# Performance work log

Hardware: AMD Instinct MI355X
Metric: run time of the kernel (lower is better)

Reference implementation:

```python
import jax, jax.numpy as jnp
import numpy as np

DIM_K = 64
DIM_V = 64
MODEL_DIM = 1024


def setup_inputs() -> dict:
    key = jax.random.key(0)
    ks = jax.random.split(key, 9)
    B, T, C = 4, 4096, MODEL_DIM
    scale = 1.0 / np.sqrt(C)
    return {
        "Q": jax.random.normal(ks[0], (B, T, C), dtype=jnp.float32),
        "K": jax.random.normal(ks[1], (B, T, C), dtype=jnp.float32),
        "V": jax.random.normal(ks[2], (B, T, C), dtype=jnp.float32),
        "Wq": jax.random.normal(ks[3], (C, DIM_K), dtype=jnp.float32) * scale,
        "bq": jax.random.normal(ks[4], (DIM_K,), dtype=jnp.float32) * 0.02,
        "Wk": jax.random.normal(ks[5], (C, DIM_K), dtype=jnp.float32) * scale,
        "bk": jax.random.normal(ks[6], (DIM_K,), dtype=jnp.float32) * 0.02,
        "Wv": jax.random.normal(ks[7], (C, DIM_V), dtype=jnp.float32) * scale,
        "bv": jax.random.normal(ks[8], (DIM_V,), dtype=jnp.float32) * 0.02,
    }


def reference(Q, K, V, Wq, bq, Wk, bk, Wv, bv):
    # Linear projections: [B,T,C] @ [C,dk] -> [B,T,dk]
    q = jnp.einsum("btc,cd->btd", Q, Wq) + bq
    k = jnp.einsum("btc,cd->btd", K, Wk) + bk
    v = jnp.einsum("btc,cd->btd", V, Wv) + bv
    T = q.shape[1]
    # Scaled dot-product scores [B,T,T], causal mask, softmax (dropout p=0 -> identity)
    scores = jnp.einsum("bqd,bkd->bqk", q, k) / jnp.sqrt(jnp.float32(DIM_K))
    causal = jnp.tril(jnp.ones((T, T), dtype=bool))
    scores = jnp.where(causal, scores, -jnp.inf)
    weights = jax.nn.softmax(scores, axis=-1)
    return jnp.einsum("bqk,bkd->bqd", weights, v)
```

## Files before the change

### kernel.cpp

```cpp
#include <hip/hip_runtime.h>
#include <hip/hip_bf16.h>
#include <cstdint>
#include <cstddef>


typedef __attribute__((ext_vector_type(8))) short short8;
typedef __attribute__((ext_vector_type(4))) float f32x4;
typedef __attribute__((ext_vector_type(4))) unsigned int uint4v;
typedef __attribute__((ext_vector_type(4))) unsigned short ushort4v;
typedef unsigned short ushort;

#define MFMA16x16x32(A,B,C) __builtin_amdgcn_mfma_f32_16x16x32_bf16((A),(B),(C),0,0,0)

static __device__ __forceinline__ unsigned pack2_bf16(float f0, float f1){
  unsigned u0 = __builtin_bit_cast(unsigned, f0) + 0x8000u;
  unsigned u1 = __builtin_bit_cast(unsigned, f1) + 0x8000u;
  return __builtin_amdgcn_perm(u1, u0, 0x07060302u);
}
static __device__ __forceinline__ unsigned short bf16u(float f){
  return (unsigned short)((__builtin_bit_cast(unsigned, f) + 0x8000u) >> 16);
}
static __device__ __forceinline__ short8 cvt8(f32x4 a, f32x4 b){
  union { unsigned u[4]; short8 s; } r;
  r.u[0] = pack2_bf16(a[0], a[1]);
  r.u[1] = pack2_bf16(a[2], a[3]);
  r.u[2] = pack2_bf16(b[0], b[1]);
  r.u[3] = pack2_bf16(b[2], b[3]);
  return r.s;
}
static __device__ __forceinline__ float fast_exp2(float x){
  float r; asm("v_exp_f32 %0, %1" : "=v"(r) : "v"(x)); return r;
}
static __device__ __forceinline__ float fast_rcp(float x){
  float r; asm("v_rcp_f32 %0, %1" : "=v"(r) : "v"(x)); return r;
}
static __device__ __forceinline__ void gl_lds16(const ushort* g, ushort* l){
  __builtin_amdgcn_global_load_lds(
      (const __attribute__((address_space(1))) void*)g,
      (__attribute__((address_space(3))) void*)l, 16, 0, 0);
}

__global__ __launch_bounds__(256) void pack_w(
    const float* __restrict__ Wq, const float* __restrict__ Wk,
    const float* __restrict__ Wv, unsigned short* __restrict__ Wp,
    float* __restrict__ out, float* __restrict__ Lbuf)
{
  int t = blockIdx.x * 256 + threadIdx.x;
  if (t < 24576){
    int lane = t & 63, nf = (t >> 6) & 3, cc = (t >> 8) & 31, p = t >> 13;
    int qd = lane >> 4, l = lane & 15;
    const float* W = (p == 0) ? Wq : ((p == 1) ? Wk : Wv);
    const float* src = W + (size_t)(cc * 32 + qd * 8) * 64 + nf * 16 + l;
    uint4v u;
    #pragma unroll
    for (int j = 0; j < 4; ++j)
      u[j] = pack2_bf16(src[(2 * j) * 64], src[(2 * j + 1) * 64]);
    *(uint4v*)(Wp + (size_t)t * 8) = u;
  }
  const f32x4 z = (f32x4){0.f, 0.f, 0.f, 0.f};
  f32x4* o4 = (f32x4*)out;
  f32x4* l4 = (f32x4*)Lbuf;
  for (int i = t; i < 262144 + 4096; i += 65536){
    if (i < 262144) o4[i] = z;
    else l4[i - 262144] = z;
  }
}

__global__ __launch_bounds__(256) void proj_gemm(
    const float* __restrict__ Qx, const float* __restrict__ Kx, const float* __restrict__ Vx,
    const float* __restrict__ bqp, const float* __restrict__ bkp, const float* __restrict__ bvp,
    const unsigned short* __restrict__ Wp,
    unsigned short* __restrict__ qb, unsigned short* __restrict__ kb,
    unsigned short* __restrict__ vt)
{
  const int tid = threadIdx.x;
  const int lane = tid & 63, wid = tid >> 6;
  const int qd = lane >> 4, l = lane & 15;
  const int p = blockIdx.y;
  const float* X = (p == 0) ? Qx : ((p == 1) ? Kx : Vx);
  const float* bias = (p == 0) ? bqp : ((p == 1) ? bkp : bvp);
  const unsigned short* W = Wp + (size_t)p * 65536;

  const int row0 = blockIdx.x * 64 + wid * 16;
  const float* xa = X + (size_t)(row0 + l) * 1024 + qd * 8;
  const unsigned short* wb = W + (size_t)lane * 8;

  f32x4 acc[4];
  #pragma unroll
  for (int nf = 0; nf < 4; ++nf) acc[nf] = (f32x4){0.f, 0.f, 0.f, 0.f};

  #pragma unroll 4
  for (int cc = 0; cc < 32; ++cc){
    f32x4 al = *(const f32x4*)(xa + cc * 32);
    f32x4 ah = *(const f32x4*)(xa + cc * 32 + 4);
    const unsigned short* wc = wb + (size_t)cc * 2048;
    short8 b0 = *(const short8*)(wc);
    short8 b1 = *(const short8*)(wc + 512);
    short8 b2 = *(const short8*)(wc + 1024);
    short8 b3 = *(const short8*)(wc + 1536);
    short8 a = cvt8(al, ah);
    acc[0] = MFMA16x16x32(a, b0, acc[0]);
    acc[1] = MFMA16x16x32(a, b1, acc[1]);
    acc[2] = MFMA16x16x32(a, b2, acc[2]);
    acc[3] = MFMA16x16x32(a, b3, acc[3]);
  }

  if (p == 2){
    int tg = row0 + qd * 4;
    int b = tg >> 12, tl = tg & 4095;
    #pragma unroll
    for (int nf = 0; nf < 4; ++nf){
      float bb = bias[nf * 16 + l];
      ushort4v pk;
      #pragma unroll
      for (int r = 0; r < 4; ++r) pk[r] = bf16u(acc[nf][r] + bb);
      *(ushort4v*)(vt + ((size_t)b * 64 + nf * 16 + l) * 4096 + tl) = pk;
    }
  } else {
    unsigned short* o = (p == 0) ? qb : kb;
    #pragma unroll
    for (int nf = 0; nf < 4; ++nf){
      float bb = bias[nf * 16 + l];
      #pragma unroll
      for (int r = 0; r < 4; ++r){
        int row = row0 + qd * 4 + r;
        o[(size_t)row * 64 + nf * 16 + l] = bf16u(acc[nf][r] + bb);
      }
    }
  }
}

#define K1 0.18033688011112042f

__global__ __launch_bounds__(256) void flash_split(
    const ushort* __restrict__ qb, const ushort* __restrict__ kb,
    const ushort* __restrict__ vt, float* __restrict__ out,
    float* __restrict__ Lbuf)
{
  __shared__ ushort Ks[2][4096];
  __shared__ ushort Vs[2][4096];
  __shared__ ushort pbuf[4][16 * 40];

  const int tid = threadIdx.x;
  const int lane = tid & 63, wid = tid >> 6;
  const int qd = lane >> 4, l = lane & 15;
  const int lw = l & 7;

  int bidx = (int)blockIdx.x;
  const int batch = bidx & 3;
  int j = 287 - (bidx >> 2);
  int g = 0;
  while (j >= 4 * (g + 1) * (g + 2)) ++g;
  int j2 = j - 4 * g * (g + 1);
  int tq = j2 / (g + 1);
  int s = j2 - tq * (g + 1);
  const int q0b = (8 * g + tq) * 64;
  const int kvstart = s * 512;
  const int kvend = min(kvstart + 512, q0b + 64);
  const int q0w = q0b + wid * 16;

  const ushort* kbB = kb + (size_t)batch * 262144;
  const ushort* vtB = vt + (size_t)batch * 262144;

  const ushort* qrow = qb + ((size_t)(batch * 4096 + q0w + l)) * 64 + qd * 8;
  short8 Qf0 = *(const short8*)(qrow);
  short8 Qf1 = *(const short8*)(qrow + 32);

  const f32x4 Zc = (f32x4){0.f, 0.f, 0.f, 0.f};
  f32x4 Oc[4] = {Zc, Zc, Zc, Zc};
  f32x4 Lacc = Zc;
  short8 onesf;
  #pragma unroll
  for (int i = 0; i < 8; ++i) onesf[i] = (short)0x3F80;

  ushort* pw = &pbuf[wid][0];
  ushort* pwr = pw + qd * 160 + l;
  const ushort* prd = pw + l * 40 + qd * 8;

#define STAGE(BB, KVC) do{                                                     \
    int r8_ = lane >> 3, sw_ = ((lane & 7) ^ r8_) << 3;                        \
    int rA_ = wid * 8 + r8_;                                                   \
    const ushort* gk_ = kbB + (size_t)((KVC) + rA_) * 64 + sw_;                \
    gl_lds16(gk_,            &Ks[BB][wid * 512]);                              \
    gl_lds16(gk_ + 32 * 64,  &Ks[BB][2048 + wid * 512]);                       \
    const ushort* gv_ = vtB + (size_t)rA_ * 4096 + (KVC) + sw_;                \
    gl_lds16(gv_,              &Vs[BB][wid * 512]);                            \
    gl_lds16(gv_ + 32 * 4096,  &Vs[BB][2048 + wid * 512]);                     \
  } while (0)

#define CHUNK(BB, ROFF, KVG) do{                                               \
    if ((KVG) < q0w + 16){                                                     \
      const ushort* KsB_ = &Ks[BB][0];                                         \
      const ushort* VsB_ = &Vs[BB][0];                                         \
      short8 k0_ = *(const short8*)(KsB_ + (l + (ROFF)) * 64 + ((qd ^ lw) << 3));        \
      short8 k1_ = *(const short8*)(KsB_ + (l + (ROFF)) * 64 + (((qd + 4) ^ lw) << 3));  \
      short8 k2_ = *(const short8*)(KsB_ + (l + 16 + (ROFF)) * 64 + ((qd ^ lw) << 3));   \
      short8 k3_ = *(const short8*)(KsB_ + (l + 16 + (ROFF)) * 64 + (((qd + 4) ^ lw) << 3)); \
      f32x4 s0_ = MFMA16x16x32(Qf0, k0_, Zc);                                  \
      s0_ = MFMA16x16x32(Qf1, k1_, s0_);                                       \
      f32x4 s1_ = MFMA16x16x32(Qf0, k2_, Zc);                                  \
      s1_ = MFMA16x16x32(Qf1, k3_, s1_);                                       \
      float p0_[4], p1_[4];                                                    \
      _Pragma("unroll")                                                        \
      for (int r = 0; r < 4; ++r){                                             \
        p0_[r] = fast_exp2(s0_[r] * K1);                                       \
        p1_[r] = fast_exp2(s1_[r] * K1);                                       \
      }                                                                        \
      if ((KVG) + 31 > q0w){                                                   \
        _Pragma("unroll")                                                      \
        for (int r = 0; r < 4; ++r){                                           \
          int q_ = q0w + qd * 4 + r;                                           \
          if ((KVG) + l > q_) p0_[r] = 0.f;                                    \
          if ((KVG) + 16 + l > q_) p1_[r] = 0.f;                               \
        }                                                                      \
      }                                                                        \
      _Pragma("unroll")                                                        \
      for (int r = 0; r < 4; ++r){                                             \
        pwr[r * 40] = bf16u(p0_[r]);                                           \
        pwr[r * 40 + 16] = bf16u(p1_[r]);                                      \
      }                                                                        \
      short8 Pf_ = *(const short8*)(prd);                                      \
      int vs_ = ((qd + ((ROFF) >> 3)) ^ lw) << 3;                              \
      short8 v0_ = *(const short8*)(VsB_ + (l     ) * 64 + vs_);               \
      short8 v1_ = *(const short8*)(VsB_ + (l + 16) * 64 + vs_);               \
      short8 v2_ = *(const short8*)(VsB_ + (l + 32) * 64 + vs_);               \
      short8 v3_ = *(const short8*)(VsB_ + (l + 48) * 64 + vs_);               \
      Lacc = MFMA16x16x32(Pf_, onesf, Lacc);                                   \
      Oc[0] = MFMA16x16x32(Pf_, v0_, Oc[0]);                                   \
      Oc[1] = MFMA16x16x32(Pf_, v1_, Oc[1]);                                   \
      Oc[2] = MFMA16x16x32(Pf_, v2_, Oc[2]);                                   \
      Oc[3] = MFMA16x16x32(Pf_, v3_, Oc[3]);                                   \
    }                                                                          \
  } while (0)

  const int nst = (kvend - kvstart) >> 6;
  STAGE(0, kvstart);
  __syncthreads();
  int kvc = kvstart;
  for (int it = 0; it < nst; ++it){
    int bb = it & 1;
    if (it + 1 < nst) STAGE(bb ^ 1, kvc + 64);
    CHUNK(bb, 0, kvc);
    CHUNK(bb, 32, kvc + 32);
    __syncthreads();
    kvc += 64;
  }
#undef STAGE
#undef CHUNK

  float* ob = out + ((size_t)(batch * 4096 + q0w + qd * 4)) * 64 + l;
  #pragma unroll
  for (int nf = 0; nf < 4; ++nf)
    #pragma unroll
    for (int r = 0; r < 4; ++r)
      atomicAdd(&ob[(size_t)r * 64 + nf * 16], Oc[nf][r]);
  if (l == 0){
    float* lb = Lbuf + batch * 4096 + q0w + qd * 4;
    #pragma unroll
    for (int r = 0; r < 4; ++r) atomicAdd(&lb[r], Lacc[r]);
  }
}

__global__ __launch_bounds__(256) void normalize(
    float* __restrict__ out, const float* __restrict__ Lbuf)
{
  int idx = blockIdx.x * 256 + threadIdx.x;
  f32x4 v = ((f32x4*)out)[idx];
  float inv = fast_rcp(Lbuf[idx >> 4]);
  v[0] *= inv; v[1] *= inv; v[2] *= inv; v[3] *= inv;
  ((f32x4*)out)[idx] = v;
}

extern "C" void kernel_launch(void* const* d_in, const int* in_sizes, int n_in,
                              void* d_out, int out_size, void* d_ws, size_t ws_size,
                              hipStream_t stream)
{
  const float* Q  = (const float*)d_in[0];
  const float* K  = (const float*)d_in[1];
  const float* V  = (const float*)d_in[2];
  const float* Wq = (const float*)d_in[3];
  const float* bq = (const float*)d_in[4];
  const float* Wk = (const float*)d_in[5];
  const float* bk = (const float*)d_in[6];
  const float* Wv = (const float*)d_in[7];
  const float* bv = (const float*)d_in[8];
  float* out = (float*)d_out;

  unsigned short* qb   = (unsigned short*)d_ws;
  unsigned short* kbuf = qb + (size_t)16384 * 64;
  unsigned short* vtp  = kbuf + (size_t)16384 * 64;
  unsigned short* Wp   = vtp + (size_t)16384 * 64;
  float* Lbuf = (float*)(Wp + (size_t)3 * 65536);

  pack_w<<<256, 256, 0, stream>>>(Wq, Wk, Wv, Wp, out, Lbuf);
  proj_gemm<<<dim3(256, 3), 256, 0, stream>>>(Q, K, V, bq, bk, bv, Wp, qb, kbuf, vtp);
  flash_split<<<1152, 256, 0, stream>>>(qb, kbuf, vtp, out, Lbuf);
  normalize<<<1024, 256, 0, stream>>>(out, Lbuf);
}
```

Measured before the change: 254.7 us.

## Stage projection inputs through LDS with double-buffered async loads; unroll flash loop by two

The projection GEMM now copies X tiles into swizzled, double-buffered LDS using global_load_lds and prefetches the next chunk of packed weights into registers. Explicit vmcnt waits overlap each load with the MFMAs on the current chunk. The goal is to hide global memory latency in this bandwidth-heavy fp32 input read. In the flash kernel the ping-pong buffers become separate static arrays and the loop is unrolled by two, so buffer selection is resolved at compile time and no longer needs runtime indexing. The tradeoff is more LDS and register pressure in proj_gemm, and the hand-written waitcnt counts must match the exact number of outstanding loads.

```diff
diff --git a/kernel.cpp b/kernel.cpp
--- a/kernel.cpp
+++ b/kernel.cpp
@@ -34,7 +34,7 @@
 static __device__ __forceinline__ float fast_rcp(float x){
   float r; asm("v_rcp_f32 %0, %1" : "=v"(r) : "v"(x)); return r;
 }
-static __device__ __forceinline__ void gl_lds16(const ushort* g, ushort* l){
+static __device__ __forceinline__ void gl_lds16(const void* g, void* l){
   __builtin_amdgcn_global_load_lds(
       (const __attribute__((address_space(1))) void*)g,
       (__attribute__((address_space(3))) void*)l, 16, 0, 0);
@@ -73,6 +73,9 @@
     unsigned short* __restrict__ qb, unsigned short* __restrict__ kb,
     unsigned short* __restrict__ vt)
 {
+  __shared__ float Xs0[4096];
+  __shared__ float Xs1[4096];
+
   const int tid = threadIdx.x;
   const int lane = tid & 63, wid = tid >> 6;
   const int qd = lane >> 4, l = lane & 15;
@@ -82,28 +85,90 @@
   const unsigned short* W = Wp + (size_t)p * 65536;
 
   const int row0 = blockIdx.x * 64 + wid * 16;
-  const float* xa = X + (size_t)(row0 + l) * 1024 + qd * 8;
+  const float* Xrow = X + (size_t)row0 * 1024;
   const unsigned short* wb = W + (size_t)lane * 8;
+
+  float* s0 = Xs0 + wid * 1024;
+  float* s1 = Xs1 + wid * 1024;
+  const float* r0 = s0 + l * 64;
+  const float* r1 = s1 + l * 64;
 
   f32x4 acc[4];
   #pragma unroll
   for (int nf = 0; nf < 4; ++nf) acc[nf] = (f32x4){0.f, 0.f, 0.f, 0.f};
 
-  #pragma unroll 4
-  for (int cc = 0; cc < 32; ++cc){
-    f32x4 al = *(const f32x4*)(xa + cc * 32);
-    f32x4 ah = *(const f32x4*)(xa + cc * 32 + 4);
-    const unsigned short* wc = wb + (size_t)cc * 2048;
-    short8 b0 = *(const short8*)(wc);
-    short8 b1 = *(const short8*)(wc + 512);
-    short8 b2 = *(const short8*)(wc + 1024);
-    short8 b3 = *(const short8*)(wc + 1536);
-    short8 a = cvt8(al, ah);
-    acc[0] = MFMA16x16x32(a, b0, acc[0]);
-    acc[1] = MFMA16x16x32(a, b1, acc[1]);
-    acc[2] = MFMA16x16x32(a, b2, acc[2]);
-    acc[3] = MFMA16x16x32(a, b3, acc[3]);
-  }
+  short8 wA0, wA1, wA2, wA3, wA4, wA5, wA6, wA7;
+  short8 wB0, wB1, wB2, wB3, wB4, wB5, wB6, wB7;
+
+#define PSTAGE(DST, CK) do{                                                    \
+    _Pragma("unroll")                                                          \
+    for (int j_ = 0; j_ < 4; ++j_){                                            \
+      int rr_ = j_ * 4 + qd;                                    \
+      int ss_ = l ^ rr_;                                  \
+      gl_lds16(Xrow + (size_t)rr_ * 1024 + (CK) * 64 + (ss_ << 2),             \
+               (DST) + j_ * 256);                                              \
+    }                                                                          \
+  } while (0)
+
+#define WLOADM(S, CK) do{                                                      \
+    const unsigned short* wc_ = wb + (size_t)(CK) * 4096;                      \
+    w##S##0 = *(const short8*)(wc_);                                           \
+    w##S##1 = *(const short8*)(wc_ + 512);                                     \
+    w##S##2 = *(const short8*)(wc_ + 1024);                                    \
+    w##S##3 = *(const short8*)(wc_ + 1536);                                    \
+    w##S##4 = *(const short8*)(wc_ + 2048);                                    \
+    w##S##5 = *(const short8*)(wc_ + 2560);                                    \
+    w##S##6 = *(const short8*)(wc_ + 3072);                                    \
+    w##S##7 = *(const short8*)(wc_ + 3584);                                    \
+  } while (0)
+
+#define PCOMP(RD, S) do{                                                       \
+    {                                                                          \
+      int sb_ = qd * 2;                                                        \
+      f32x4 al_ = *(const f32x4*)((RD) + ((sb_ ^ l) << 2));                    \
+      f32x4 ah_ = *(const f32x4*)((RD) + (((sb_ + 1) ^ l) << 2));              \
+      short8 a_ = cvt8(al_, ah_);                                              \
+      acc[0] = MFMA16x16x32(a_, w##S##0, acc[0]);                              \
+      acc[1] = MFMA16x16x32(a_, w##S##1, acc[1]);                              \
+      acc[2] = MFMA16x16x32(a_, w##S##2, acc[2]);                              \
+      acc[3] = MFMA16x16x32(a_, w##S##3, acc[3]);                              \
+    }                                                                          \
+    {                                                                          \
+      int sb_ = 8 + qd * 2;                                                    \
+      f32x4 al_ = *(const f32x4*)((RD) + ((sb_ ^ l) << 2));                    \
+      f32x4 ah_ = *(const f32x4*)((RD) + (((sb_ + 1) ^ l) << 2));              \
+      short8 a_ = cvt8(al_, ah_);                                              \
+      acc[0] = MFMA16x16x32(a_, w##S##4, acc[0]);                              \
+      acc[1] = MFMA16x16x32(a_, w##S##5, acc[1]);                              \
+      acc[2] = MFMA16x16x32(a_, w##S##6, acc[2]);                              \
+      acc[3] = MFMA16x16x32(a_, w##S##7, acc[3]);                              \
+    }                                                                          \
+  } while (0)
+
+#define VW12 do{ asm volatile("s_waitcnt vmcnt(12)" ::: "memory");             \
+                 __builtin_amdgcn_sched_barrier(0); } while (0)
+#define VW0  do{ asm volatile("s_waitcnt vmcnt(0)"  ::: "memory");             \
+                 __builtin_amdgcn_sched_barrier(0); } while (0)
+
+  PSTAGE(s0, 0);
+  WLOADM(A, 0);
+  #pragma unroll
+  for (int h = 0; h < 16; ++h){
+    if ((h & 1) == 0){
+      if (h + 1 < 16){ PSTAGE(s1, h + 1); WLOADM(B, h + 1); VW12; }
+      else           { VW0; }
+      PCOMP(r0, A);
+    } else {
+      if (h + 1 < 16){ PSTAGE(s0, h + 1); WLOADM(A, h + 1); VW12; }
+      else           { VW0; }
+      PCOMP(r1, B);
+    }
+  }
+#undef PSTAGE
+#undef WLOADM
+#undef PCOMP
+#undef VW12
+#undef VW0
 
   if (p == 2){
     int tg = row0 + qd * 4;
@@ -137,8 +202,10 @@
     const ushort* __restrict__ vt, float* __restrict__ out,
     float* __restrict__ Lbuf)
 {
-  __shared__ ushort Ks[2][4096];
-  __shared__ ushort Vs[2][4096];
+  __shared__ ushort Ks0[4096];
+  __shared__ ushort Ks1[4096];
+  __shared__ ushort Vs0[4096];
+  __shared__ ushort Vs1[4096];
   __shared__ ushort pbuf[4][16 * 40];
 
   const int tid = threadIdx.x;
@@ -177,21 +244,21 @@
   ushort* pwr = pw + qd * 160 + l;
   const ushort* prd = pw + l * 40 + qd * 8;
 
-#define STAGE(BB, KVC) do{                                                     \
+#define STAGE(KA, VA, KVC) do{                                                 \
     int r8_ = lane >> 3, sw_ = ((lane & 7) ^ r8_) << 3;                        \
     int rA_ = wid * 8 + r8_;                                                   \
     const ushort* gk_ = kbB + (size_t)((KVC) + rA_) * 64 + sw_;                \
-    gl_lds16(gk_,            &Ks[BB][wid * 512]);                              \
-    gl_lds16(gk_ + 32 * 64,  &Ks[BB][2048 + wid * 512]);                       \
+    gl_lds16(gk_,            &(KA)[wid * 512]);                                \
+    gl_lds16(gk_ + 32 * 64,  &(KA)[2048 + wid * 512]);                         \
     const ushort* gv_ = vtB + (size_t)rA_ * 4096 + (KVC) + sw_;                \
-    gl_lds16(gv_,              &Vs[BB][wid * 512]);                            \
-    gl_lds16(gv_ + 32 * 4096,  &Vs[BB][2048 + wid * 512]);                     \
-  } while (0)
-
-#define CHUNK(BB, ROFF, KVG) do{                                               \
+    gl_lds16(gv_,              &(VA)[wid * 512]);                              \
+    gl_lds16(gv_ + 32 * 4096,  &(VA)[2048 + wid * 512]);                       \
+  } while (0)
+
+#define CHUNK(KA, VA, ROFF, KVG) do{                                           \
     if ((KVG) < q0w + 16){                                                     \
-      const ushort* KsB_ = &Ks[BB][0];                                         \
-      const ushort* VsB_ = &Vs[BB][0];                                         \
+      const ushort* KsB_ = &(KA)[0];                                           \
+      const ushort* VsB_ = &(VA)[0];                                           \
       short8 k0_ = *(const short8*)(KsB_ + (l + (ROFF)) * 64 + ((qd ^ lw) << 3));        \
       short8 k1_ = *(const short8*)(KsB_ + (l + (ROFF)) * 64 + (((qd + 4) ^ lw) << 3));  \
       short8 k2_ = *(const short8*)(KsB_ + (l + 16 + (ROFF)) * 64 + ((qd ^ lw) << 3));   \
@@ -234,16 +301,24 @@
   } while (0)
 
   const int nst = (kvend - kvstart) >> 6;
-  STAGE(0, kvstart);
+  int kvc = kvstart;
+  STAGE(Ks0, Vs0, kvc);
   __syncthreads();
-  int kvc = kvstart;
-  for (int it = 0; it < nst; ++it){
-    int bb = it & 1;
-    if (it + 1 < nst) STAGE(bb ^ 1, kvc + 64);
-    CHUNK(bb, 0, kvc);
-    CHUNK(bb, 32, kvc + 32);
+  int it = 0;
+  for (; it + 2 <= nst; it += 2){
+    STAGE(Ks1, Vs1, kvc + 64);
+    CHUNK(Ks0, Vs0, 0, kvc);
+    CHUNK(Ks0, Vs0, 32, kvc + 32);
     __syncthreads();
-    kvc += 64;
+    if (it + 2 < nst) STAGE(Ks0, Vs0, kvc + 128);
+    CHUNK(Ks1, Vs1, 0, kvc + 64);
+    CHUNK(Ks1, Vs1, 32, kvc + 96);
+    __syncthreads();
+    kvc += 128;
+  }
+  if (it < nst){
+    CHUNK(Ks0, Vs0, 0, kvc);
+    CHUNK(Ks0, Vs0, 32, kvc + 32);
   }
 #undef STAGE
 #undef CHUNK
```

Measured after the change: 254.5 us. Within noise of the previous version (-0.1%).

## Split projection K-loop across two waves and unroll flash double-buffer loop

Applied to the files above, without the earlier changes.

The projection GEMM now launches 512 threads per block, with two waves per 16-row tile each covering half of the 1024-wide reduction. Partial sums are combined through shared memory before the bias, bf16 conversion and store. This doubles the number of waves available to hide the latency of the fp32 input loads, at the cost of a block barrier and an LDS round trip. Separately, the flash kernel's double-buffer loop is unrolled by two with statically named K/V buffers, removing dynamic buffer indexing, and gains a tail iteration for an odd stage count.

```diff
diff --git a/kernel.cpp b/kernel.cpp
--- a/kernel.cpp
+++ b/kernel.cpp
@@ -34,7 +34,7 @@
 static __device__ __forceinline__ float fast_rcp(float x){
   float r; asm("v_rcp_f32 %0, %1" : "=v"(r) : "v"(x)); return r;
 }
-static __device__ __forceinline__ void gl_lds16(const ushort* g, ushort* l){
+static __device__ __forceinline__ void gl_lds16(const void* g, void* l){
   __builtin_amdgcn_global_load_lds(
       (const __attribute__((address_space(1))) void*)g,
       (__attribute__((address_space(3))) void*)l, 16, 0, 0);
@@ -66,22 +66,25 @@
   }
 }
 
-__global__ __launch_bounds__(256) void proj_gemm(
+__global__ __launch_bounds__(512, 6) void proj_gemm(
     const float* __restrict__ Qx, const float* __restrict__ Kx, const float* __restrict__ Vx,
     const float* __restrict__ bqp, const float* __restrict__ bkp, const float* __restrict__ bvp,
     const unsigned short* __restrict__ Wp,
     unsigned short* __restrict__ qb, unsigned short* __restrict__ kb,
     unsigned short* __restrict__ vt)
 {
+  __shared__ float cs[4][64][16];
+
   const int tid = threadIdx.x;
   const int lane = tid & 63, wid = tid >> 6;
+  const int kh = wid & 1, rt = wid >> 1;
   const int qd = lane >> 4, l = lane & 15;
   const int p = blockIdx.y;
   const float* X = (p == 0) ? Qx : ((p == 1) ? Kx : Vx);
   const float* bias = (p == 0) ? bqp : ((p == 1) ? bkp : bvp);
   const unsigned short* W = Wp + (size_t)p * 65536;
 
-  const int row0 = blockIdx.x * 64 + wid * 16;
+  const int row0 = blockIdx.x * 64 + rt * 16;
   const float* xa = X + (size_t)(row0 + l) * 1024 + qd * 8;
   const unsigned short* wb = W + (size_t)lane * 8;
 
@@ -89,8 +92,9 @@
   #pragma unroll
   for (int nf = 0; nf < 4; ++nf) acc[nf] = (f32x4){0.f, 0.f, 0.f, 0.f};
 
+  const int cc0 = kh * 16;
   #pragma unroll 4
-  for (int cc = 0; cc < 32; ++cc){
+  for (int cc = cc0; cc < cc0 + 16; ++cc){
     f32x4 al = *(const f32x4*)(xa + cc * 32);
     f32x4 ah = *(const f32x4*)(xa + cc * 32 + 4);
     const unsigned short* wc = wb + (size_t)cc * 2048;
@@ -105,26 +109,43 @@
     acc[3] = MFMA16x16x32(a, b3, acc[3]);
   }
 
-  if (p == 2){
-    int tg = row0 + qd * 4;
-    int b = tg >> 12, tl = tg & 4095;
+  if (kh == 1){
+    float* dst = &cs[rt][lane][0];
+    #pragma unroll
+    for (int nf = 0; nf < 4; ++nf)
+      *(f32x4*)(dst + nf * 4) = acc[nf];
+  }
+  __syncthreads();
+  if (kh == 0){
+    const float* src = &cs[rt][lane][0];
     #pragma unroll
     for (int nf = 0; nf < 4; ++nf){
-      float bb = bias[nf * 16 + l];
-      ushort4v pk;
+      f32x4 o = *(const f32x4*)(src + nf * 4);
+      acc[nf][0] += o[0]; acc[nf][1] += o[1];
+      acc[nf][2] += o[2]; acc[nf][3] += o[3];
+    }
+
+    if (p == 2){
+      int tg = row0 + qd * 4;
+      int b = tg >> 12, tl = tg & 4095;
       #pragma unroll
-      for (int r = 0; r < 4; ++r) pk[r] = bf16u(acc[nf][r] + bb);
-      *(ushort4v*)(vt + ((size_t)b * 64 + nf * 16 + l) * 4096 + tl) = pk;
-    }
-  } else {
-    unsigned short* o = (p == 0) ? qb : kb;
-    #pragma unroll
-    for (int nf = 0; nf < 4; ++nf){
-      float bb = bias[nf * 16 + l];
+      for (int nf = 0; nf < 4; ++nf){
+        float bb = bias[nf * 16 + l];
+        ushort4v pk;
+        #pragma unroll
+        for (int r = 0; r < 4; ++r) pk[r] = bf16u(acc[nf][r] + bb);
+        *(ushort4v*)(vt + ((size_t)b * 64 + nf * 16 + l) * 4096 + tl) = pk;
+      }
+    } else {
+      unsigned short* o = (p == 0) ? qb : kb;
       #pragma unroll
-      for (int r = 0; r < 4; ++r){
-        int row = row0 + qd * 4 + r;
-        o[(size_t)row * 64 + nf * 16 + l] = bf16u(acc[nf][r] + bb);
+      for (int nf = 0; nf < 4; ++nf){
+        float bb = bias[nf * 16 + l];
+        #pragma unroll
+        for (int r = 0; r < 4; ++r){
+          int row = row0 + qd * 4 + r;
+          o[(size_t)row * 64 + nf * 16 + l] = bf16u(acc[nf][r] + bb);
+        }
       }
     }
   }
@@ -137,8 +158,10 @@
     const ushort* __restrict__ vt, float* __restrict__ out,
     float* __restrict__ Lbuf)
 {
-  __shared__ ushort Ks[2][4096];
-  __shared__ ushort Vs[2][4096];
+  __shared__ ushort Ks0[4096];
+  __shared__ ushort Ks1[4096];
+  __shared__ ushort Vs0[4096];
+  __shared__ ushort Vs1[4096];
   __shared__ ushort pbuf[4][16 * 40];
 
   const int tid = threadIdx.x;
@@ -177,21 +200,21 @@
   ushort* pwr = pw + qd * 160 + l;
   const ushort* prd = pw + l * 40 + qd * 8;
 
-#define STAGE(BB, KVC) do{                                                     \
+#define STAGE(KA, VA, KVC) do{                                                 \
     int r8_ = lane >> 3, sw_ = ((lane & 7) ^ r8_) << 3;                        \
     int rA_ = wid * 8 + r8_;                                                   \
     const ushort* gk_ = kbB + (size_t)((KVC) + rA_) * 64 + sw_;                \
-    gl_lds16(gk_,            &Ks[BB][wid * 512]);                              \
-    gl_lds16(gk_ + 32 * 64,  &Ks[BB][2048 + wid * 512]);                       \
+    gl_lds16(gk_,            &(KA)[wid * 512]);                                \
+    gl_lds16(gk_ + 32 * 64,  &(KA)[2048 + wid * 512]);                         \
     const ushort* gv_ = vtB + (size_t)rA_ * 4096 + (KVC) + sw_;                \
-    gl_lds16(gv_,              &Vs[BB][wid * 512]);                            \
-    gl_lds16(gv_ + 32 * 4096,  &Vs[BB][2048 + wid * 512]);                     \
+    gl_lds16(gv_,              &(VA)[wid * 512]);                              \
+    gl_lds16(gv_ + 32 * 4096,  &(VA)[2048 + wid * 512]);                       \
   } while (0)
 
-#define CHUNK(BB, ROFF, KVG) do{                                               \
+#define CHUNK(KA, VA, ROFF, KVG) do{                                           \
     if ((KVG) < q0w + 16){                                                     \
-      const ushort* KsB_ = &Ks[BB][0];                                         \
-      const ushort* VsB_ = &Vs[BB][0];                                         \
+      const ushort* KsB_ = &(KA)[0];                                           \
+      const ushort* VsB_ = &(VA)[0];                                           \
       short8 k0_ = *(const short8*)(KsB_ + (l + (ROFF)) * 64 + ((qd ^ lw) << 3));        \
       short8 k1_ = *(const short8*)(KsB_ + (l + (ROFF)) * 64 + (((qd + 4) ^ lw) << 3));  \
       short8 k2_ = *(const short8*)(KsB_ + (l + 16 + (ROFF)) * 64 + ((qd ^ lw) << 3));   \
@@ -234,16 +257,24 @@
   } while (0)
 
   const int nst = (kvend - kvstart) >> 6;
-  STAGE(0, kvstart);
+  int kvc = kvstart;
+  STAGE(Ks0, Vs0, kvc);
   __syncthreads();
-  int kvc = kvstart;
-  for (int it = 0; it < nst; ++it){
-    int bb = it & 1;
-    if (it + 1 < nst) STAGE(bb ^ 1, kvc + 64);
-    CHUNK(bb, 0, kvc);
-    CHUNK(bb, 32, kvc + 32);
+  int it = 0;
+  for (; it + 2 <= nst; it += 2){
+    STAGE(Ks1, Vs1, kvc + 64);
+    CHUNK(Ks0, Vs0, 0, kvc);
+    CHUNK(Ks0, Vs0, 32, kvc + 32);
     __syncthreads();
-    kvc += 64;
+    if (it + 2 < nst) STAGE(Ks0, Vs0, kvc + 128);
+    CHUNK(Ks1, Vs1, 0, kvc + 64);
+    CHUNK(Ks1, Vs1, 32, kvc + 96);
+    __syncthreads();
+    kvc += 128;
+  }
+  if (it < nst){
+    CHUNK(Ks0, Vs0, 0, kvc);
+    CHUNK(Ks0, Vs0, 32, kvc + 32);
   }
 #undef STAGE
 #undef CHUNK
@@ -293,7 +324,7 @@
   float* Lbuf = (float*)(Wp + (size_t)3 * 65536);
 
   pack_w<<<256, 256, 0, stream>>>(Wq, Wk, Wv, Wp, out, Lbuf);
-  proj_gemm<<<dim3(256, 3), 256, 0, stream>>>(Q, K, V, bq, bk, bv, Wp, qb, kbuf, vtp);
+  proj_gemm<<<dim3(256, 3), 512, 0, stream>>>(Q, K, V, bq, bk, bv, Wp, qb, kbuf, vtp);
   flash_split<<<1152, 256, 0, stream>>>(qb, kbuf, vtp, out, Lbuf);
   normalize<<<1024, 256, 0, stream>>>(out, Lbuf);
 }
```

Result: faster. 249.2 us (-2.2%).
